# Kernel optimization log

Measured on AMD Instinct MI355X. Metric: run time of the kernel, lower is better.

The kernel has to match this reference:

```python
import jax, jax.numpy as jnp
import numpy as np

B, N, V, E_PER = 64, 512, 64, 16384
IN, H, OUT = 128, 256, 10
TOTAL_N = B * N
E = B * E_PER


def _lin_init(key, fan_in, fan_out):
    return jax.random.normal(key, (fan_in, fan_out), jnp.float32) * (1.0 / np.sqrt(fan_in))


def setup_inputs() -> dict:
    key = jax.random.key(0)
    ks = jax.random.split(key, 16)
    x = jax.random.normal(ks[0], (TOTAL_N, IN), jnp.float32)
    # within-graph random edges, offset to global node ids
    off = (jnp.arange(B, dtype=jnp.int32) * N)[:, None]
    edge_src = (jax.random.randint(ks[1], (B, E_PER), 0, N, dtype=jnp.int32) + off).reshape(-1)
    edge_dst = (jax.random.randint(ks[2], (B, E_PER), 0, N, dtype=jnp.int32) + off).reshape(-1)
    inp = dict(
        x=x, edge_src=edge_src, edge_dst=edge_dst,
        W_emb=_lin_init(ks[3], IN, H), b_emb=jnp.zeros((H,), jnp.float32),
        W_gcn=_lin_init(ks[4], H, H), b_gcn=jnp.zeros((H,), jnp.float32),
        aW1=_lin_init(ks[5], H, H), ab1=jnp.zeros((H,), jnp.float32),
        aW2=_lin_init(ks[6], H, H), ab2=jnp.zeros((H,), jnp.float32),
        vW1=_lin_init(ks[7], H, H), vb1=jnp.zeros((H,), jnp.float32),
        vW2=_lin_init(ks[8], H, H), vb2=jnp.zeros((H,), jnp.float32),
        mW1=_lin_init(ks[9], H, H), mb1=jnp.zeros((H,), jnp.float32),
        mW2=_lin_init(ks[10], H, OUT), mb2=jnp.zeros((OUT,), jnp.float32),
        edge_weights=jnp.ones((B, N, V), jnp.float32) / V,  # uniform init
    )
    return inp


def reference(x, edge_src, edge_dst, W_emb, b_emb, W_gcn, b_gcn,
              aW1, ab1, aW2, ab2, vW1, vb1, vW2, vb2,
              mW1, mb1, mW2, mb2, edge_weights):
    # node embedding
    h = x @ W_emb + b_emb                                   # [BN, H]
    # GCNConv with symmetric normalization + self loops (PyG semantics)
    hw = h @ W_gcn                                          # [BN, H]
    deg = 1.0 + jax.ops.segment_sum(jnp.ones((E,), jnp.float32), edge_dst, num_segments=TOTAL_N)
    dinv = jax.lax.rsqrt(deg)
    coef = (dinv[edge_src] * dinv[edge_dst])[:, None]
    agg = jax.ops.segment_sum(hw[edge_src] * coef, edge_dst, num_segments=TOTAL_N)
    agg = agg + hw / deg[:, None]                           # self-loop term (norm = 1/deg)
    h = jax.nn.relu(agg + b_gcn)
    g = h.reshape(B, N, H)                                  # per-graph node features
    # affinity MLP + cosine similarity to graph prototype
    t = jax.nn.relu(g @ aW1 + ab1) @ aW2 + ab2              # [B, N, H]
    proto = t.mean(axis=1)                                  # [B, H]
    eps = 1e-8
    tn = jnp.maximum(jnp.linalg.norm(t, axis=-1), eps)      # [B, N]
    pn = jnp.maximum(jnp.linalg.norm(proto, axis=-1), eps)  # [B]
    sim = jnp.einsum('bnh,bh->bn', t, proto) / (tn * pn[:, None])
    att = 0.5 * (1.0 + sim)                                 # [B, N]
    mw = edge_weights * att[:, :, None]                     # [B, N, V]
    rs = mw.sum(axis=-1, keepdims=True)
    mw = mw / jnp.where(rs == 0.0, 1.0, rs)                 # row-normalize (top_k=None path)
    # weighted scatter of node features into virtual nodes
    vn = jnp.einsum('bnv,bnh->bvh', mw, g)                  # [B, V, H]
    vn = jax.nn.relu(vn @ vW1 + vb1) @ vW2 + vb2
    gf = vn.mean(axis=1)                                    # [B, H]
    out = jax.nn.relu(gf @ mW1 + mb1) @ mW2 + mb2           # [B, OUT]
    return out
```

## Files before the change

kernel.cpp:

```cpp
#include <hip/hip_runtime.h>
#include <hip/hip_bf16.h>

#define DEVINL __device__ __forceinline__

typedef unsigned short u16;
typedef short v8s   __attribute__((ext_vector_type(8)));
typedef float v4f   __attribute__((ext_vector_type(4)));
typedef u16   v4u16 __attribute__((ext_vector_type(4)));
typedef short v4s16 __attribute__((ext_vector_type(4)));
typedef int   v4i   __attribute__((ext_vector_type(4)));

constexpr int Bg      = 64;
constexpr int Nn      = 512;
constexpr int Vv      = 64;
constexpr int IND     = 128;
constexpr int Hd      = 256;
constexpr int OUTD    = 10;
constexpr int TOTAL_N = Bg * Nn;
constexpr int NE      = Bg * 16384;
constexpr int E_PER   = 16384;

DEVINL u16 f2bf(float f) {
    unsigned u = __float_as_uint(f);
    u += 0x7FFF + ((u >> 16) & 1);
    return (u16)(u >> 16);
}
DEVINL float bf2f(u16 s) { return __uint_as_float(((unsigned)s) << 16); }

DEVINL void ld4f(const float* p, float o[4]) {
    float4 v = *(const float4*)p;
    o[0] = v.x; o[1] = v.y; o[2] = v.z; o[3] = v.w;
}
DEVINL void ld4f(const u16* p, float o[4]) {
    v4u16 v = *(const v4u16*)p;
    o[0] = bf2f(v[0]); o[1] = bf2f(v[1]); o[2] = bf2f(v[2]); o[3] = bf2f(v[3]);
}
DEVINL void stC(float* C, size_t idx, float v) { C[idx] = v; }
DEVINL void stC(u16* C, size_t idx, float v)   { C[idx] = f2bf(v); }

__global__ __launch_bounds__(1024) void k_csr(const int* __restrict__ esrc,
                                              const int* __restrict__ edst,
                                              int2* __restrict__ csr,
                                              int* __restrict__ rowstart,
                                              float* __restrict__ dinv,
                                              float* __restrict__ srow) {
    __shared__ int   cnt[512];
    __shared__ int   cur[512];
    __shared__ float dv[512];
    __shared__ float sfs[512];
    __shared__ u16   dlc[E_PER];
    int g = blockIdx.x;
    int tid = threadIdx.x;
    if (tid < 512) { cnt[tid] = 0; sfs[tid] = 0.f; }
    __syncthreads();
    const int base = g * E_PER;
    const v4i* edst4 = (const v4i*)(edst + base);
    const v4i* esrc4 = (const v4i*)(esrc + base);
#pragma unroll
    for (int i = 0; i < E_PER / 4096; i++) {
        int idx = i * 1024 + tid;
        v4i d4 = edst4[idx];
#pragma unroll
        for (int c = 0; c < 4; c++) {
            int dl = d4[c] & 511;
            dlc[idx * 4 + c] = (u16)dl;
            atomicAdd(&cnt[dl], 1);
        }
    }
    __syncthreads();
    if (tid < 512) cur[tid] = cnt[tid];
    __syncthreads();
    for (int off = 1; off < 512; off <<= 1) {
        int v = 0;
        if (tid < 512 && tid >= off) v = cur[tid - off];
        __syncthreads();
        if (tid < 512) cur[tid] += v;
        __syncthreads();
    }
    if (tid < 512) {
        int excl = cur[tid] - cnt[tid];
        rowstart[g * 512 + tid] = base + excl;
        float di = rsqrtf((float)(cnt[tid] + 1));
        dv[tid] = di;
        dinv[g * 512 + tid] = di;
        cur[tid] = excl;
    }
    if (g == 0 && tid == 0) rowstart[TOTAL_N] = NE;
    __syncthreads();
#pragma unroll
    for (int i = 0; i < E_PER / 4096; i++) {
        int idx = i * 1024 + tid;
        v4i s4 = esrc4[idx];
#pragma unroll
        for (int c = 0; c < 4; c++) {
            int s = s4[c];
            int dl = dlc[idx * 4 + c];
            float coef = dv[s & 511] * dv[dl];
            int pos = atomicAdd(&cur[dl], 1);
            int2 rec;
            rec.x = s;
            rec.y = __float_as_int(coef);
            csr[base + pos] = rec;
            atomicAdd(&sfs[dl], coef);
        }
    }
    __syncthreads();
    if (tid < 512) srow[g * 512 + tid] = sfs[tid] + dv[tid] * dv[tid];
}

struct WtArgs {
    const float* src[5];
    u16* dst[5];
    const float* b_emb;
    float* b12;
};
__global__ __launch_bounds__(256) void k_wt(WtArgs a) {
    int bid = blockIdx.x;
    int t = threadIdx.x;
    if (bid == 80) {
        const float* Wg = a.src[0];
        float a0 = 0.f, a1 = 0.f, a2 = 0.f, a3 = 0.f;
        for (int k = 0; k < IND; k += 4) {
            a0 += a.b_emb[k]     * Wg[(size_t)k * 256 + t];
            a1 += a.b_emb[k + 1] * Wg[(size_t)(k + 1) * 256 + t];
            a2 += a.b_emb[k + 2] * Wg[(size_t)(k + 2) * 256 + t];
            a3 += a.b_emb[k + 3] * Wg[(size_t)(k + 3) * 256 + t];
        }
        a.b12[t] = (a0 + a1) + (a2 + a3);
        return;
    }
    int mi = bid / 16, tile = bid % 16;
    int k0 = (tile & 3) * 64, n0 = (tile >> 2) * 64;
    const float* src = a.src[mi];
    u16* dst = a.dst[mi];
    __shared__ float T[64][65];
#pragma unroll
    for (int j = 0; j < 16; j++) {
        int idx = t + 256 * j;
        int r = idx >> 6, c = idx & 63;
        T[c][r] = src[(size_t)(k0 + r) * 256 + n0 + c];
    }
    __syncthreads();
#pragma unroll
    for (int j = 0; j < 16; j++) {
        int idx = t + 256 * j;
        int nr = idx >> 6, kc = idx & 63;
        dst[(size_t)(n0 + nr) * 256 + k0 + kc] = f2bf(T[nr][kc]);
    }
}

__global__ __launch_bounds__(256) void k_w12(const float* __restrict__ W_emb,
                                             const float* __restrict__ W_gcn,
                                             u16* __restrict__ wt_12) {
    __shared__ float WgT[4][256];
    int n0 = blockIdx.x * 4;
    int t = threadIdx.x;
    {
        float4 f = *(const float4*)(W_gcn + (size_t)t * Hd + n0);
        WgT[0][t] = f.x; WgT[1][t] = f.y; WgT[2][t] = f.z; WgT[3][t] = f.w;
    }
    __syncthreads();
    int k = t & 127, c = (t >> 7) * 2;
    const float4* we = (const float4*)(W_emb + (size_t)k * Hd);
    const float* g0 = &WgT[c][0];
    const float* g1 = &WgT[c + 1][0];
    float a00 = 0.f, a01 = 0.f, a10 = 0.f, a11 = 0.f;
#pragma unroll
    for (int h4 = 0; h4 < 64; h4 += 2) {
        float4 w0 = we[h4], w1 = we[h4 + 1];
        int h = h4 * 4;
        a00 += w0.x * g0[h]     + w0.y * g0[h + 1] + w0.z * g0[h + 2] + w0.w * g0[h + 3];
        a01 += w0.x * g1[h]     + w0.y * g1[h + 1] + w0.z * g1[h + 2] + w0.w * g1[h + 3];
        a10 += w1.x * g0[h + 4] + w1.y * g0[h + 5] + w1.z * g0[h + 6] + w1.w * g0[h + 7];
        a11 += w1.x * g1[h + 4] + w1.y * g1[h + 5] + w1.z * g1[h + 6] + w1.w * g1[h + 7];
    }
    wt_12[(size_t)(n0 + c)     * IND + k] = f2bf(a00 + a10);
    wt_12[(size_t)(n0 + c + 1) * IND + k] = f2bf(a01 + a11);
}

template <typename TA, typename TC>
__global__ __launch_bounds__(256) void k_mfma_gemm(const TA* __restrict__ A,
                                                   const u16* __restrict__ Wt,
                                                   const float* __restrict__ bias,
                                                   const float* __restrict__ srow,
                                                   const float* __restrict__ b12v,
                                                   TC* __restrict__ C,
                                                   u16* __restrict__ gt,
                                                   int M, int K, int relu) {
    constexpr int LDK = 72;
    __shared__ short As[128 * LDK];
    __shared__ short Bs[128 * LDK];
    int tid  = threadIdx.x;
    int row0 = blockIdx.y * 128, col0 = blockIdx.x * 128;
    int lane = tid & 63, wid = tid >> 6;
    int wm = (wid >> 1) * 64, wn = (wid & 1) * 64;
    int q = lane >> 4, r = lane & 15;
    v4f acc[4][4];
#pragma unroll
    for (int i = 0; i < 4; i++)
#pragma unroll
        for (int j = 0; j < 4; j++) acc[i][j] = (v4f){0.f, 0.f, 0.f, 0.f};
    int sm = tid >> 1, sk = (tid & 1) * 32;
    for (int k0 = 0; k0 < K; k0 += 64) {
        const TA* ap  = A  + (size_t)(row0 + sm) * K + k0 + sk;
        const u16* bp = Wt + (size_t)(col0 + sm) * K + k0 + sk;
        short* adst = &As[sm * LDK + sk];
        short* bdst = &Bs[sm * LDK + sk];
#pragma unroll
        for (int i = 0; i < 8; i++) {
            float o[4];
            ld4f(ap + 4 * i, o);
            v4s16 pa;
            pa[0] = (short)f2bf(o[0]); pa[1] = (short)f2bf(o[1]);
            pa[2] = (short)f2bf(o[2]); pa[3] = (short)f2bf(o[3]);
            *(v4s16*)(adst + 4 * i) = pa;
            *(v4u16*)(bdst + 4 * i) = *(const v4u16*)(bp + 4 * i);
        }
        __syncthreads();
#pragma unroll
        for (int ks = 0; ks < 64; ks += 32) {
            v8s af[4], bfr[4];
#pragma unroll
            for (int i = 0; i < 4; i++)
                af[i] = *(const v8s*)&As[(wm + i * 16 + r) * LDK + ks + q * 8];
#pragma unroll
            for (int j = 0; j < 4; j++)
                bfr[j] = *(const v8s*)&Bs[(wn + j * 16 + r) * LDK + ks + q * 8];
#pragma unroll
            for (int i = 0; i < 4; i++)
#pragma unroll
                for (int j = 0; j < 4; j++)
                    acc[i][j] = __builtin_amdgcn_mfma_f32_16x16x32_bf16(af[i], bfr[j], acc[i][j], 0, 0, 0);
        }
        __syncthreads();
    }
#pragma unroll
    for (int i = 0; i < 4; i++) {
#pragma unroll
        for (int j = 0; j < 4; j++) {
            int col = col0 + wn + j * 16 + r;
            float bcol = bias ? bias[col] : 0.f;
            float b12c = b12v ? b12v[col] : 0.f;
            int rowb = row0 + wm + i * 16 + q * 4;
            v4u16 gvec;
#pragma unroll
            for (int rg = 0; rg < 4; rg++) {
                int row = rowb + rg;
                float v = acc[i][j][rg] + bcol;
                if (srow) v += srow[row] * b12c;
                if (relu) v = fmaxf(v, 0.f);
                stC(C, (size_t)row * 256 + col, v);
                gvec[rg] = f2bf(v);
            }
            if (gt)
                *(v4u16*)&gt[(((size_t)(rowb >> 9) * 256 + col) << 9) + (rowb & 511)] = gvec;
        }
    }
}

__global__ __launch_bounds__(256) void k_xbf(const float* __restrict__ x,
                                             u16* __restrict__ xbf) {
    int idx = blockIdx.x * 256 + threadIdx.x;
    float4 f = *(const float4*)&x[(size_t)idx * 4];
    v4u16 p;
    p[0] = f2bf(f.x); p[1] = f2bf(f.y); p[2] = f2bf(f.z); p[3] = f2bf(f.w);
    *(v4u16*)&xbf[(size_t)idx * 4] = p;
}

__global__ __launch_bounds__(64) void k_aggx(const float* __restrict__ x,
                                             const u16* __restrict__ xbf,
                                             const int* __restrict__ rowstart,
                                             const int2* __restrict__ csr,
                                             const float* __restrict__ dinv,
                                             u16* __restrict__ xa) {
    __shared__ int   loff[64];
    __shared__ float lcoef[64];
    int node = ((blockIdx.x & 7) << 12) | (blockIdx.x >> 3);
    int ch = threadIdx.x;
    int ch2 = ch * 2;
    float di = dinv[node];
    float invdeg = di * di;
    float2 xv = *(const float2*)&x[(size_t)node * IND + ch2];
    float sa = xv.x * invdeg, sb = xv.y * invdeg;
    float a0=0.f,a1=0.f,a2=0.f,a3=0.f,a4=0.f,a5=0.f,a6=0.f,a7=0.f;
    float b0=0.f,b1=0.f,b2=0.f,b3=0.f,b4=0.f,b5=0.f,b6=0.f,b7=0.f;
    int rs0 = rowstart[node], rs1 = rowstart[node + 1];
    for (int base = rs0; base < rs1; base += 64) {
        int e = base + ch;
        if (e < rs1) {
            int2 rr = csr[e];
            loff[ch]  = rr.x << 7;
            lcoef[ch] = __int_as_float(rr.y);
        }
        __syncthreads();
        int m = min(64, rs1 - base);
        int i = 0;
        for (; i + 8 <= m; i += 8) {
            unsigned u0 = *(const unsigned*)&xbf[loff[i    ] + ch2];
            unsigned u1 = *(const unsigned*)&xbf[loff[i + 1] + ch2];
            unsigned u2 = *(const unsigned*)&xbf[loff[i + 2] + ch2];
            unsigned u3 = *(const unsigned*)&xbf[loff[i + 3] + ch2];
            unsigned u4 = *(const unsigned*)&xbf[loff[i + 4] + ch2];
            unsigned u5 = *(const unsigned*)&xbf[loff[i + 5] + ch2];
            unsigned u6 = *(const unsigned*)&xbf[loff[i + 6] + ch2];
            unsigned u7 = *(const unsigned*)&xbf[loff[i + 7] + ch2];
            float c0 = lcoef[i],     c1 = lcoef[i + 1], c2 = lcoef[i + 2], c3 = lcoef[i + 3];
            float c4 = lcoef[i + 4], c5 = lcoef[i + 5], c6 = lcoef[i + 6], c7 = lcoef[i + 7];
            a0 += __uint_as_float(u0 << 16) * c0; b0 += __uint_as_float(u0 & 0xffff0000u) * c0;
            a1 += __uint_as_float(u1 << 16) * c1; b1 += __uint_as_float(u1 & 0xffff0000u) * c1;
            a2 += __uint_as_float(u2 << 16) * c2; b2 += __uint_as_float(u2 & 0xffff0000u) * c2;
            a3 += __uint_as_float(u3 << 16) * c3; b3 += __uint_as_float(u3 & 0xffff0000u) * c3;
            a4 += __uint_as_float(u4 << 16) * c4; b4 += __uint_as_float(u4 & 0xffff0000u) * c4;
            a5 += __uint_as_float(u5 << 16) * c5; b5 += __uint_as_float(u5 & 0xffff0000u) * c5;
            a6 += __uint_as_float(u6 << 16) * c6; b6 += __uint_as_float(u6 & 0xffff0000u) * c6;
            a7 += __uint_as_float(u7 << 16) * c7; b7 += __uint_as_float(u7 & 0xffff0000u) * c7;
        }
        for (; i < m; i++) {
            unsigned u = *(const unsigned*)&xbf[loff[i] + ch2];
            float c = lcoef[i];
            a0 += __uint_as_float(u << 16) * c;
            b0 += __uint_as_float(u & 0xffff0000u) * c;
        }
        __syncthreads();
    }
    float ra = ((a0 + a1) + (a2 + a3)) + ((a4 + a5) + (a6 + a7)) + sa;
    float rb = ((b0 + b1) + (b2 + b3)) + ((b4 + b5) + (b6 + b7)) + sb;
    unsigned packed = ((unsigned)f2bf(rb) << 16) | (unsigned)f2bf(ra);
    *(unsigned*)&xa[(size_t)node * IND + ch2] = packed;
}

__global__ __launch_bounds__(1024) void k_proto(const u16* __restrict__ t,
                                                float* __restrict__ proto,
                                                float* __restrict__ pn) {
    __shared__ float part[4][256];
    __shared__ float red[256];
    int b = blockIdx.x;
    int tid = threadIdx.x;
    int st = tid >> 8, ch = tid & 255;
    int n0 = st * 128;
    float s0 = 0.f, s1 = 0.f, s2 = 0.f, s3 = 0.f;
    for (int n = n0; n < n0 + 128; n += 4) {
        s0 += bf2f(t[(size_t)(b * Nn + n)     * Hd + ch]);
        s1 += bf2f(t[(size_t)(b * Nn + n + 1) * Hd + ch]);
        s2 += bf2f(t[(size_t)(b * Nn + n + 2) * Hd + ch]);
        s3 += bf2f(t[(size_t)(b * Nn + n + 3) * Hd + ch]);
    }
    part[st][ch] = (s0 + s1) + (s2 + s3);
    __syncthreads();
    if (tid < 256) {
        float p = (part[0][ch] + part[1][ch] + part[2][ch] + part[3][ch]) * (1.f / (float)Nn);
        proto[b * Hd + ch] = p;
        red[ch] = p * p;
    }
    __syncthreads();
    for (int off = 128; off > 0; off >>= 1) {
        if (tid < off) red[tid] += red[tid + off];
        __syncthreads();
    }
    if (tid == 0) pn[b] = fmaxf(sqrtf(red[0]), 1e-8f);
}

__global__ __launch_bounds__(256) void k_att(const u16* __restrict__ t,
                                             const float* __restrict__ proto,
                                             const float* __restrict__ pn,
                                             const float* __restrict__ ew,
                                             float* __restrict__ scale) {
    int tid = threadIdx.x;
    int lane = tid & 63, widx = tid >> 6;
    int node = blockIdx.x * 4 + widx;
    int b = node >> 9;
    v4u16 tv4 = *(const v4u16*)&t[(size_t)node * Hd + lane * 4];
    float4 pv4 = *(const float4*)&proto[b * Hd + lane * 4];
    float t0 = bf2f(tv4[0]), t1 = bf2f(tv4[1]), t2 = bf2f(tv4[2]), t3 = bf2f(tv4[3]);
    float dot = t0 * pv4.x + t1 * pv4.y + t2 * pv4.z + t3 * pv4.w;
    float sq  = t0 * t0 + t1 * t1 + t2 * t2 + t3 * t3;
    float wv  = ew[(size_t)node * Vv + lane];
#pragma unroll
    for (int off = 32; off > 0; off >>= 1) {
        dot += __shfl_xor(dot, off);
        sq  += __shfl_xor(sq, off);
        wv  += __shfl_xor(wv, off);
    }
    if (lane == 0) {
        float tn  = fmaxf(sqrtf(sq), 1e-8f);
        float sim = dot / (tn * pn[b]);
        float att = 0.5f * (1.f + sim);
        float rs  = att * wv;
        float den = (rs == 0.f) ? 1.f : rs;
        scale[node] = att / den;
    }
}

__global__ __launch_bounds__(256) void k_mwt(const float* __restrict__ ew,
                                             const float* __restrict__ scale,
                                             u16* __restrict__ mwT) {
    __shared__ short T[64][72];
    int bid = blockIdx.x;
    int b = bid >> 3, n0 = (bid & 7) * 64;
    int t = threadIdx.x;
    int nl = t >> 2, vseg = (t & 3) * 16;
    float s = scale[b * 512 + n0 + nl];
    const float* src = ew + ((size_t)(b * 512 + n0 + nl)) * Vv + vseg;
#pragma unroll
    for (int c = 0; c < 4; c++) {
        float4 f = *(const float4*)(src + c * 4);
        T[vseg + c * 4 + 0][nl] = (short)f2bf(f.x * s);
        T[vseg + c * 4 + 1][nl] = (short)f2bf(f.y * s);
        T[vseg + c * 4 + 2][nl] = (short)f2bf(f.z * s);
        T[vseg + c * 4 + 3][nl] = (short)f2bf(f.w * s);
    }
    __syncthreads();
    int v = t >> 2, seg = (t & 3) * 16;
    u16* dst = mwT + ((size_t)(b * Vv + v)) * 512 + n0 + seg;
    *(v8s*)(dst)     = *(const v8s*)&T[v][seg];
    *(v8s*)(dst + 8) = *(const v8s*)&T[v][seg + 8];
}

__global__ __launch_bounds__(256) void k_vn_mfma(const u16* __restrict__ mwT,
                                                 const u16* __restrict__ gT,
                                                 u16* __restrict__ vn) {
    int virt = blockIdx.x;
    int xcd = virt & 7, j = virt >> 3;
    int b = xcd * 8 + (j >> 2), h0 = (j & 3) * 64;
    int tid = threadIdx.x;
    int lane = tid & 63, wid = tid >> 6;
    int wm = (wid >> 1) * 32, wn = (wid & 1) * 32;
    int q = lane >> 4, r = lane & 15;
    const u16* a0p = mwT + (size_t)(b * Vv + wm + r) * 512 + q * 8;
    const u16* a1p = a0p + 16 * 512;
    const u16* b0p = gT + (size_t)(b * Hd + h0 + wn + r) * 512 + q * 8;
    const u16* b1p = b0p + 16 * 512;
    v4f acc00 = (v4f){0.f,0.f,0.f,0.f}, acc01 = acc00, acc10 = acc00, acc11 = acc00;
#pragma unroll
    for (int k0 = 0; k0 < Nn; k0 += 32) {
        v8s a0 = *(const v8s*)(a0p + k0);
        v8s a1 = *(const v8s*)(a1p + k0);
        v8s b0 = *(const v8s*)(b0p + k0);
        v8s b1 = *(const v8s*)(b1p + k0);
        acc00 = __builtin_amdgcn_mfma_f32_16x16x32_bf16(a0, b0, acc00, 0, 0, 0);
        acc01 = __builtin_amdgcn_mfma_f32_16x16x32_bf16(a0, b1, acc01, 0, 0, 0);
        acc10 = __builtin_amdgcn_mfma_f32_16x16x32_bf16(a1, b0, acc10, 0, 0, 0);
        acc11 = __builtin_amdgcn_mfma_f32_16x16x32_bf16(a1, b1, acc11, 0, 0, 0);
    }
    v4f accs[2][2] = {{acc00, acc01}, {acc10, acc11}};
#pragma unroll
    for (int i = 0; i < 2; i++)
#pragma unroll
        for (int jj = 0; jj < 2; jj++) {
            int col = h0 + wn + jj * 16 + r;
#pragma unroll
            for (int rg = 0; rg < 4; rg++) {
                int v = wm + i * 16 + q * 4 + rg;
                vn[(size_t)(b * Vv + v) * Hd + col] = f2bf(accs[i][jj][rg]);
            }
        }
}

__global__ __launch_bounds__(256) void k_head(const float* __restrict__ vn2,
                                              const float* __restrict__ mW1,
                                              const float* __restrict__ mb1,
                                              const float* __restrict__ mW2,
                                              const float* __restrict__ mb2,
                                              float* __restrict__ out) {
    __shared__ float gfs[256];
    __shared__ float zs[256];
    int b = blockIdx.x, t = threadIdx.x;
    float s = 0.f;
    for (int v = 0; v < Vv; v++) s += vn2[(size_t)(b * Vv + v) * Hd + t];
    gfs[t] = s * (1.f / (float)Vv);
    __syncthreads();
    float z = mb1[t];
    for (int k = 0; k < Hd; k++) z += gfs[k] * mW1[k * Hd + t];
    zs[t] = fmaxf(z, 0.f);
    __syncthreads();
    if (t < OUTD) {
        float o = mb2[t];
        for (int ch = 0; ch < Hd; ch++) o += zs[ch] * mW2[ch * OUTD + t];
        out[b * OUTD + t] = o;
    }
}

extern "C" void kernel_launch(void* const* d_in, const int* in_sizes, int n_in,
                              void* d_out, int out_size, void* d_ws, size_t ws_size,
                              hipStream_t stream) {
    const float* x     = (const float*)d_in[0];
    const int*   esrc  = (const int*)d_in[1];
    const int*   edst  = (const int*)d_in[2];
    const float* W_emb = (const float*)d_in[3];
    const float* b_emb = (const float*)d_in[4];
    const float* W_gcn = (const float*)d_in[5];
    const float* b_gcn = (const float*)d_in[6];
    const float* aW1   = (const float*)d_in[7];
    const float* ab1   = (const float*)d_in[8];
    const float* aW2   = (const float*)d_in[9];
    const float* ab2   = (const float*)d_in[10];
    const float* vW1   = (const float*)d_in[11];
    const float* vb1   = (const float*)d_in[12];
    const float* vW2   = (const float*)d_in[13];
    const float* vb2   = (const float*)d_in[14];
    const float* mW1   = (const float*)d_in[15];
    const float* mb1   = (const float*)d_in[16];
    const float* mW2   = (const float*)d_in[17];
    const float* mb2   = (const float*)d_in[18];
    const float* ew    = (const float*)d_in[19];
    float* out = (float*)d_out;

    char* w = (char*)d_ws;
    auto alloc = [&](size_t bytes) -> void* {
        void* p = (void*)w;
        w += (bytes + 255) & ~(size_t)255;
        return p;
    };
    int*   rowstart = (int*)  alloc((TOTAL_N + 1) * 4);
    float* dinv     = (float*)alloc(TOTAL_N * 4);
    int2*  csr      = (int2*) alloc((size_t)NE * 8);
    u16*   xbf      = (u16*)  alloc((size_t)TOTAL_N * IND * 2);
    u16*   xa_bf    = (u16*)  alloc((size_t)TOTAL_N * IND * 2);
    float* srow     = (float*)alloc(TOTAL_N * 4);
    u16*   g_bf     = (u16*)  alloc((size_t)TOTAL_N * Hd * 2);
    u16*   gT_bf    = (u16*)  alloc((size_t)TOTAL_N * Hd * 2);
    u16*   mwT_bf   = (u16*)  alloc((size_t)Bg * Vv * Nn * 2);
    u16*   t1_bf    = (u16*)  alloc((size_t)TOTAL_N * Hd * 2);
    u16*   t_bf     = (u16*)  alloc((size_t)TOTAL_N * Hd * 2);
    u16*   vn_bf    = (u16*)  alloc((size_t)Bg * Vv * Hd * 2);
    u16*   vtmp_bf  = (u16*)  alloc((size_t)Bg * Vv * Hd * 2);
    float* vn2      = (float*)alloc((size_t)Bg * Vv * Hd * 4);
    float* proto    = (float*)alloc(Bg * Hd * 4);
    float* pn       = (float*)alloc(Bg * 4);
    float* scale    = (float*)alloc(TOTAL_N * 4);
    float* b12      = (float*)alloc(Hd * 4);
    u16*   wt_gcn   = (u16*)  alloc((size_t)Hd * Hd * 2);
    u16*   wt_a1    = (u16*)  alloc((size_t)Hd * Hd * 2);
    u16*   wt_a2    = (u16*)  alloc((size_t)Hd * Hd * 2);
    u16*   wt_v1    = (u16*)  alloc((size_t)Hd * Hd * 2);
    u16*   wt_v2    = (u16*)  alloc((size_t)Hd * Hd * 2);
    u16*   wt_12    = (u16*)  alloc((size_t)Hd * IND * 2);

    k_csr<<<Bg, 1024, 0, stream>>>(esrc, edst, csr, rowstart, dinv, srow);

    k_xbf<<<TOTAL_N * IND / 4 / 256, 256, 0, stream>>>(x, xbf);

    WtArgs wa;
    wa.src[0] = W_gcn; wa.dst[0] = wt_gcn;
    wa.src[1] = aW1;   wa.dst[1] = wt_a1;
    wa.src[2] = aW2;   wa.dst[2] = wt_a2;
    wa.src[3] = vW1;   wa.dst[3] = wt_v1;
    wa.src[4] = vW2;   wa.dst[4] = wt_v2;
    wa.b_emb = b_emb;  wa.b12 = b12;
    k_wt<<<81, 256, 0, stream>>>(wa);

    k_w12<<<Hd / 4, 256, 0, stream>>>(W_emb, W_gcn, wt_12);

    k_aggx<<<TOTAL_N, 64, 0, stream>>>(x, xbf, rowstart, csr, dinv, xa_bf);

    k_mfma_gemm<u16, u16><<<dim3(2, TOTAL_N / 128), 256, 0, stream>>>(
        xa_bf, wt_12, b_gcn, srow, b12, g_bf, gT_bf, TOTAL_N, IND, 1);

    k_mfma_gemm<u16, u16><<<dim3(2, TOTAL_N / 128), 256, 0, stream>>>(
        g_bf, wt_a1, ab1, nullptr, nullptr, t1_bf, nullptr, TOTAL_N, Hd, 1);
    k_mfma_gemm<u16, u16><<<dim3(2, TOTAL_N / 128), 256, 0, stream>>>(
        t1_bf, wt_a2, ab2, nullptr, nullptr, t_bf, nullptr, TOTAL_N, Hd, 0);

    k_proto<<<Bg, 1024, 0, stream>>>(t_bf, proto, pn);
    k_att<<<TOTAL_N / 4, 256, 0, stream>>>(t_bf, proto, pn, ew, scale);

    k_mwt<<<Bg * 8, 256, 0, stream>>>(ew, scale, mwT_bf);

    k_vn_mfma<<<Bg * 4, 256, 0, stream>>>(mwT_bf, gT_bf, vn_bf);

    k_mfma_gemm<u16, u16><<<dim3(2, (Bg * Vv) / 128), 256, 0, stream>>>(
        vn_bf, wt_v1, vb1, nullptr, nullptr, vtmp_bf, nullptr, Bg * Vv, Hd, 1);
    k_mfma_gemm<u16, float><<<dim3(2, (Bg * Vv) / 128), 256, 0, stream>>>(
        vtmp_bf, wt_v2, vb2, nullptr, nullptr, vn2, nullptr, Bg * Vv, Hd, 0);

    k_head<<<Bg, 256, 0, stream>>>(vn2, mW1, mb1, mW2, mb2, out);
}
```

Measured before the change: 293.5 us.

## Load MFMA operands directly from global memory, dropping LDS staging

New measurement: 312.3 us. +6.4%, slower.

```diff
diff --git a/kernel.cpp b/kernel.cpp
--- a/kernel.cpp
+++ b/kernel.cpp
@@ -27,14 +27,6 @@
 }
 DEVINL float bf2f(u16 s) { return __uint_as_float(((unsigned)s) << 16); }
 
-DEVINL void ld4f(const float* p, float o[4]) {
-    float4 v = *(const float4*)p;
-    o[0] = v.x; o[1] = v.y; o[2] = v.z; o[3] = v.w;
-}
-DEVINL void ld4f(const u16* p, float o[4]) {
-    v4u16 v = *(const v4u16*)p;
-    o[0] = bf2f(v[0]); o[1] = bf2f(v[1]); o[2] = bf2f(v[2]); o[3] = bf2f(v[3]);
-}
 DEVINL void stC(float* C, size_t idx, float v) { C[idx] = v; }
 DEVINL void stC(u16* C, size_t idx, float v)   { C[idx] = f2bf(v); }
 
@@ -178,61 +170,41 @@
     wt_12[(size_t)(n0 + c + 1) * IND + k] = f2bf(a01 + a11);
 }
 
-template <typename TA, typename TC>
-__global__ __launch_bounds__(256) void k_mfma_gemm(const TA* __restrict__ A,
+template <typename TC, int K>
+__global__ __launch_bounds__(256) void k_mfma_gemm(const u16* __restrict__ A,
                                                    const u16* __restrict__ Wt,
                                                    const float* __restrict__ bias,
                                                    const float* __restrict__ srow,
                                                    const float* __restrict__ b12v,
                                                    TC* __restrict__ C,
                                                    u16* __restrict__ gt,
-                                                   int M, int K, int relu) {
-    constexpr int LDK = 72;
-    __shared__ short As[128 * LDK];
-    __shared__ short Bs[128 * LDK];
+                                                   int M, int relu) {
     int tid  = threadIdx.x;
     int row0 = blockIdx.y * 128, col0 = blockIdx.x * 128;
     int lane = tid & 63, wid = tid >> 6;
     int wm = (wid >> 1) * 64, wn = (wid & 1) * 64;
     int q = lane >> 4, r = lane & 15;
+    const u16* ap0 = A  + (size_t)(row0 + wm + r) * K + q * 8;
+    const u16* bp0 = Wt + (size_t)(col0 + wn + r) * K + q * 8;
     v4f acc[4][4];
 #pragma unroll
     for (int i = 0; i < 4; i++)
 #pragma unroll
         for (int j = 0; j < 4; j++) acc[i][j] = (v4f){0.f, 0.f, 0.f, 0.f};
-    int sm = tid >> 1, sk = (tid & 1) * 32;
-    for (int k0 = 0; k0 < K; k0 += 64) {
-        const TA* ap  = A  + (size_t)(row0 + sm) * K + k0 + sk;
-        const u16* bp = Wt + (size_t)(col0 + sm) * K + k0 + sk;
-        short* adst = &As[sm * LDK + sk];
-        short* bdst = &Bs[sm * LDK + sk];
-#pragma unroll
-        for (int i = 0; i < 8; i++) {
-            float o[4];
-            ld4f(ap + 4 * i, o);
-            v4s16 pa;
-            pa[0] = (short)f2bf(o[0]); pa[1] = (short)f2bf(o[1]);
-            pa[2] = (short)f2bf(o[2]); pa[3] = (short)f2bf(o[3]);
-            *(v4s16*)(adst + 4 * i) = pa;
-            *(v4u16*)(bdst + 4 * i) = *(const v4u16*)(bp + 4 * i);
-        }
-        __syncthreads();
-#pragma unroll
-        for (int ks = 0; ks < 64; ks += 32) {
-            v8s af[4], bfr[4];
-#pragma unroll
-            for (int i = 0; i < 4; i++)
-                af[i] = *(const v8s*)&As[(wm + i * 16 + r) * LDK + ks + q * 8];
+#pragma unroll
+    for (int k0 = 0; k0 < K; k0 += 32) {
+        v8s af[4], bfr[4];
+#pragma unroll
+        for (int i = 0; i < 4; i++)
+            af[i] = *(const v8s*)(ap0 + (size_t)(i * 16) * K + k0);
+#pragma unroll
+        for (int j = 0; j < 4; j++)
+            bfr[j] = *(const v8s*)(bp0 + (size_t)(j * 16) * K + k0);
+#pragma unroll
+        for (int i = 0; i < 4; i++)
 #pragma unroll
             for (int j = 0; j < 4; j++)
-                bfr[j] = *(const v8s*)&Bs[(wn + j * 16 + r) * LDK + ks + q * 8];
-#pragma unroll
-            for (int i = 0; i < 4; i++)
-#pragma unroll
-                for (int j = 0; j < 4; j++)
-                    acc[i][j] = __builtin_amdgcn_mfma_f32_16x16x32_bf16(af[i], bfr[j], acc[i][j], 0, 0, 0);
-        }
-        __syncthreads();
+                acc[i][j] = __builtin_amdgcn_mfma_f32_16x16x32_bf16(af[i], bfr[j], acc[i][j], 0, 0, 0);
     }
 #pragma unroll
     for (int i = 0; i < 4; i++) {
@@ -553,13 +525,13 @@
 
     k_aggx<<<TOTAL_N, 64, 0, stream>>>(x, xbf, rowstart, csr, dinv, xa_bf);
 
-    k_mfma_gemm<u16, u16><<<dim3(2, TOTAL_N / 128), 256, 0, stream>>>(
-        xa_bf, wt_12, b_gcn, srow, b12, g_bf, gT_bf, TOTAL_N, IND, 1);
-
-    k_mfma_gemm<u16, u16><<<dim3(2, TOTAL_N / 128), 256, 0, stream>>>(
-        g_bf, wt_a1, ab1, nullptr, nullptr, t1_bf, nullptr, TOTAL_N, Hd, 1);
-    k_mfma_gemm<u16, u16><<<dim3(2, TOTAL_N / 128), 256, 0, stream>>>(
-        t1_bf, wt_a2, ab2, nullptr, nullptr, t_bf, nullptr, TOTAL_N, Hd, 0);
+    k_mfma_gemm<u16, IND><<<dim3(2, TOTAL_N / 128), 256, 0, stream>>>(
+        xa_bf, wt_12, b_gcn, srow, b12, g_bf, gT_bf, TOTAL_N, 1);
+
+    k_mfma_gemm<u16, Hd><<<dim3(2, TOTAL_N / 128), 256, 0, stream>>>(
+        g_bf, wt_a1, ab1, nullptr, nullptr, t1_bf, nullptr, TOTAL_N, 1);
+    k_mfma_gemm<u16, Hd><<<dim3(2, TOTAL_N / 128), 256, 0, stream>>>(
+        t1_bf, wt_a2, ab2, nullptr, nullptr, t_bf, nullptr, TOTAL_N, 0);
 
     k_proto<<<Bg, 1024, 0, stream>>>(t_bf, proto, pn);
     k_att<<<TOTAL_N / 4, 256, 0, stream>>>(t_bf, proto, pn, ew, scale);
@@ -568,10 +540,10 @@
 
     k_vn_mfma<<<Bg * 4, 256, 0, stream>>>(mwT_bf, gT_bf, vn_bf);
 
-    k_mfma_gemm<u16, u16><<<dim3(2, (Bg * Vv) / 128), 256, 0, stream>>>(
-        vn_bf, wt_v1, vb1, nullptr, nullptr, vtmp_bf, nullptr, Bg * Vv, Hd, 1);
-    k_mfma_gemm<u16, float><<<dim3(2, (Bg * Vv) / 128), 256, 0, stream>>>(
-        vtmp_bf, wt_v2, vb2, nullptr, nullptr, vn2, nullptr, Bg * Vv, Hd, 0);
+    k_mfma_gemm<u16, Hd><<<dim3(2, (Bg * Vv) / 128), 256, 0, stream>>>(
+        vn_bf, wt_v1, vb1, nullptr, nullptr, vtmp_bf, nullptr, Bg * Vv, 1);
+    k_mfma_gemm<float, Hd><<<dim3(2, (Bg * Vv) / 128), 256, 0, stream>>>(
+        vtmp_bf, wt_v2, vb2, nullptr, nullptr, vn2, nullptr, Bg * Vv, 0);
 
     k_head<<<Bg, 256, 0, stream>>>(vn2, mW1, mb1, mW2, mb2, out);
 }
```
